# Optimization experiments

Hardware: AMD Instinct MI355X
Metric: run time of the kernel (lower is better)

The kernel has to match this reference:

```python
import jax, jax.numpy as jnp
import numpy as np

N, E, IN_C, HID, OUT_C, HEADS, NUM_CLASSES = 50000, 800000, 128, 64, 64, 4, 40
NEG_SLOPE = 0.2


def _gat_conv(x, src, dst, W, a_src, a_dst, bias, heads, concat):
    # x: [N, F_in]; W: [F_in, heads*C]; a_src/a_dst: [1, heads, C]; bias: [out]
    n = x.shape[0]
    h = (x @ W).reshape(n, heads, -1)                      # [N, H, C]
    alpha_s = (h * a_src).sum(-1)                          # [N, H]
    alpha_d = (h * a_dst).sum(-1)                          # [N, H]
    e = jax.nn.leaky_relu(alpha_s[src] + alpha_d[dst], NEG_SLOPE)  # [E, H]
    # scatter-softmax over incoming edges of each dst node
    emax = jax.ops.segment_max(e, dst, num_segments=n)
    emax = jnp.where(jnp.isfinite(emax), emax, 0.0)
    ee = jnp.exp(e - emax[dst])
    denom = jax.ops.segment_sum(ee, dst, num_segments=n) + 1e-16
    w = ee / denom[dst]                                    # [E, H]
    out = jax.ops.segment_sum(h[src] * w[:, :, None], dst, num_segments=n)  # [N, H, C]
    out = out.reshape(n, -1) if concat else out.mean(axis=1)
    return out + bias


def setup_inputs() -> dict:
    key = jax.random.key(0)
    ks = jax.random.split(key, 12)
    s1 = 1.0 / np.sqrt(IN_C)
    s2 = 1.0 / np.sqrt(HID * HEADS)
    s3 = 1.0 / np.sqrt(OUT_C)
    return {
        "x": jax.random.normal(ks[0], (N, IN_C), dtype=jnp.float32),
        "edge_index": jax.random.randint(ks[1], (2, E), 0, N, dtype=jnp.int64),
        "W1": jax.random.normal(ks[2], (IN_C, HEADS * HID), dtype=jnp.float32) * s1,
        "att_src1": jax.random.normal(ks[3], (1, HEADS, HID), dtype=jnp.float32) * s1,
        "att_dst1": jax.random.normal(ks[4], (1, HEADS, HID), dtype=jnp.float32) * s1,
        "b1": jnp.zeros((HEADS * HID,), dtype=jnp.float32),
        "W2": jax.random.normal(ks[5], (HEADS * HID, OUT_C), dtype=jnp.float32) * s2,
        "att_src2": jax.random.normal(ks[6], (1, 1, OUT_C), dtype=jnp.float32) * s2,
        "att_dst2": jax.random.normal(ks[7], (1, 1, OUT_C), dtype=jnp.float32) * s2,
        "b2": jnp.zeros((OUT_C,), dtype=jnp.float32),
        "fc_w": jax.random.normal(ks[8], (OUT_C, NUM_CLASSES), dtype=jnp.float32) * s3,
        "fc_b": jnp.zeros((NUM_CLASSES,), dtype=jnp.float32),
    }


def reference(x, edge_index, W1, att_src1, att_dst1, b1, W2, att_src2, att_dst2, b2, fc_w, fc_b):
    n = x.shape[0]
    loops = jnp.arange(n, dtype=edge_index.dtype)
    ei = jnp.concatenate([edge_index, jnp.stack([loops, loops])], axis=1)  # add self-loops (PyG default)
    src, dst = ei[0], ei[1]
    h = jax.nn.relu(_gat_conv(x, src, dst, W1, att_src1, att_dst1, b1, HEADS, True))
    h = jax.nn.relu(_gat_conv(h, src, dst, W2, att_src2, att_dst2, b2, 1, False))
    # dropout p=0.01 is identity in eval mode
    pooled = h.mean(axis=0, keepdims=True)                 # global mean pool -> [1, OUT_C]
    logits = pooled @ fc_w + fc_b
    return jax.nn.log_softmax(logits, axis=1)
```

## Files before the change

kernel.cpp:

```cpp
#include <hip/hip_runtime.h>
#include <hip/hip_bf16.h>
#include <math.h>

#define NEG_SLOPE 0.2f
#define CHUNK2 2048
#define PGROUPS 32

typedef __attribute__((ext_vector_type(8))) short bf16x8;
typedef __attribute__((ext_vector_type(4))) float f32x4;
typedef __attribute__((ext_vector_type(2))) float f32x2_t;

__device__ __forceinline__ float lrelu(float a) { return a >= 0.f ? a : NEG_SLOPE * a; }
__device__ __forceinline__ unsigned short f2bu(float v) {
  unsigned u = __float_as_uint(v);
  u += 0x7fffu + ((u >> 16) & 1u);
  return (unsigned short)(u >> 16);
}
__device__ __forceinline__ unsigned char f2fp8(float v) {
  return (unsigned char)(__builtin_amdgcn_cvt_pk_fp8_f32(v, v, 0, false) & 0xFF);
}
__device__ __forceinline__ void fp8x4_dec(unsigned v, float& a, float& b, float& c, float& d) {
  f32x2_t lo = __builtin_amdgcn_cvt_pk_f32_fp8(v, false);
  f32x2_t hi = __builtin_amdgcn_cvt_pk_f32_fp8(v, true);
  a = lo.x; b = lo.y; c = hi.x; d = hi.y;
}

__global__ __launch_bounds__(256) void prep_kernel(
    const float4* __restrict__ x4, ushort4* __restrict__ xb4, int nx4,
    const float* __restrict__ W1, unsigned short* __restrict__ w1t,
    const float* __restrict__ W2, unsigned short* __restrict__ w2t,
    const int* __restrict__ ei, int* __restrict__ bhist, int E0, int Etot, int NBUCK,
    int castBlocks, int wBlocks, int histBlocks) {
  __shared__ int hsm[256];
  int t = threadIdx.x;
  if (blockIdx.x < (unsigned)castBlocks) {
    for (int i = blockIdx.x * 256 + t; i < nx4; i += castBlocks * 256) {
      float4 v = x4[i];
      xb4[i] = make_ushort4(f2bu(v.x), f2bu(v.y), f2bu(v.z), f2bu(v.w));
    }
  } else if (blockIdx.x < (unsigned)(castBlocks + wBlocks)) {
    int bid = blockIdx.x - castBlocks;
    const int tot1 = 128 * 256, tot2 = 256 * 64;
    for (int i = bid * 256 + t; i < tot1 + tot2; i += wBlocks * 256) {
      if (i < tot1) { int k = i >> 8, n = i & 255; w1t[n * 128 + k] = f2bu(W1[i]); }
      else { int j = i - tot1; int k = j >> 6, n = j & 63; w2t[n * 256 + k] = f2bu(W2[j]); }
    }
  } else {
    int bid = blockIdx.x - castBlocks - wBlocks;
    hsm[t] = 0;
    __syncthreads();
    for (int e = bid * 256 + t; e < Etot; e += histBlocks * 256) {
      int dst = (e < E0) ? ei[E0 + e] : (e - E0);
      atomicAdd(&hsm[dst >> 8], 1);
    }
    __syncthreads();
    if (t < NBUCK && hsm[t]) atomicAdd(&bhist[t], hsm[t]);
  }
}

__global__ __launch_bounds__(256) void bucket_scan_kernel(const int* __restrict__ bhist,
    int* __restrict__ bucketOff, int* __restrict__ cursor, int* __restrict__ rowptrN,
    float* __restrict__ pooled_grp, int NBUCK, int Etot) {
  __shared__ int s[256];
  int t = threadIdx.x;
  int v = (t < NBUCK) ? bhist[t] : 0;
  s[t] = v;
  __syncthreads();
  for (int off = 1; off < 256; off <<= 1) {
    int u = (t >= off) ? s[t - off] : 0;
    __syncthreads();
    s[t] += u;
    __syncthreads();
  }
  int excl = s[t] - v;
  if (t < NBUCK) { bucketOff[t] = excl; cursor[t] = excl; }
  if (t == 0) { bucketOff[NBUCK] = Etot; *rowptrN = Etot; }
  for (int i = t; i < PGROUPS * 64; i += 256) pooled_grp[i] = 0.f;
}

__device__ void gemm_tile(const unsigned short* __restrict__ A,
    const unsigned short* __restrict__ BT, unsigned char* __restrict__ C8,
    const float* __restrict__ att_s, const float* __restrict__ att_d,
    float* __restrict__ as_, float* __restrict__ ad_,
    int M, int K, int Ncol, int H, int bx, int by, char* smem) {
  unsigned short (*Al)[40] = (unsigned short (*)[40])smem;
  unsigned short (*Bt)[40] = (unsigned short (*)[40])(smem + 5120);
  float* sal = (float*)(smem + 10240);
  float* sad = (float*)(smem + 10752);
  const int tid = threadIdx.x;
  const int row0 = by * 64, col0 = bx * 64;
  const int lane = tid & 63, wave = tid >> 6;
  const int wm = wave >> 1, wn = wave & 1;
  const int l15 = lane & 15, q = lane >> 4;

  f32x4 acc[2][2] = {};

  const int rr = tid >> 2, rc = (tid & 3) * 8;

  for (int k0 = 0; k0 < K; k0 += 32) {
    ushort4 av0 = make_ushort4(0, 0, 0, 0), av1 = av0;
    if (row0 + rr < M) {
      const ushort4* ap = (const ushort4*)(A + (size_t)(row0 + rr) * K + k0 + rc);
      av0 = ap[0]; av1 = ap[1];
    }
    *(ushort4*)&Al[rr][rc] = av0;
    *(ushort4*)&Al[rr][rc + 4] = av1;
    {
      const ushort4* bp = (const ushort4*)(BT + (size_t)(col0 + rr) * K + k0 + rc);
      *(ushort4*)&Bt[rr][rc] = bp[0];
      *(ushort4*)&Bt[rr][rc + 4] = bp[1];
    }
    __syncthreads();
    bf16x8 af[2], bf[2];
#pragma unroll
    for (int mi = 0; mi < 2; mi++)
      af[mi] = *(const bf16x8*)&Al[wm * 32 + mi * 16 + l15][q * 8];
#pragma unroll
    for (int ni = 0; ni < 2; ni++)
      bf[ni] = *(const bf16x8*)&Bt[wn * 32 + ni * 16 + l15][q * 8];
#pragma unroll
    for (int mi = 0; mi < 2; mi++)
#pragma unroll
      for (int ni = 0; ni < 2; ni++)
        acc[mi][ni] = __builtin_amdgcn_mfma_f32_16x16x32_bf16(af[mi], bf[ni], acc[mi][ni], 0, 0, 0);
    __syncthreads();
  }
#pragma unroll
  for (int mi = 0; mi < 2; mi++) {
#pragma unroll
    for (int r = 0; r < 4; r++) {
      int grow = row0 + wm * 32 + mi * 16 + q * 4 + r;
      if (grow < M) {
#pragma unroll
        for (int ni = 0; ni < 2; ni++) {
          int gcol = col0 + wn * 32 + ni * 16 + l15;
          C8[(size_t)grow * Ncol + gcol] = f2fp8(acc[mi][ni][r]);
        }
      }
    }
  }
  float atts0 = att_s[col0 + wn * 32 + l15];
  float atts1 = att_s[col0 + wn * 32 + 16 + l15];
  float attd0 = att_d[col0 + wn * 32 + l15];
  float attd1 = att_d[col0 + wn * 32 + 16 + l15];
#pragma unroll
  for (int mi = 0; mi < 2; mi++) {
#pragma unroll
    for (int r = 0; r < 4; r++) {
      float vs = acc[mi][0][r] * atts0 + acc[mi][1][r] * atts1;
      float vd = acc[mi][0][r] * attd0 + acc[mi][1][r] * attd1;
#pragma unroll
      for (int off = 1; off < 16; off <<= 1) {
        vs += __shfl_xor(vs, off);
        vd += __shfl_xor(vd, off);
      }
      if (l15 == 0) {
        int rl = wm * 32 + mi * 16 + q * 4 + r;
        sal[wn * 64 + rl] = vs;
        sad[wn * 64 + rl] = vd;
      }
    }
  }
  __syncthreads();
  if (tid < 64) {
    int grow = row0 + tid;
    if (grow < M) {
      as_[(size_t)grow * H + bx] = sal[tid] + sal[64 + tid];
      ad_[(size_t)grow * H + bx] = sad[tid] + sad[64 + tid];
    }
  }
}

__global__ __launch_bounds__(256) void gemm_alpha_kernel(const unsigned short* __restrict__ A,
    const unsigned short* __restrict__ BT, unsigned char* __restrict__ C8,
    const float* __restrict__ att_s, const float* __restrict__ att_d,
    float* __restrict__ as_, float* __restrict__ ad_, int M, int K, int Ncol, int H) {
  __shared__ __align__(16) char smem[11264];
  gemm_tile(A, BT, C8, att_s, att_d, as_, ad_, M, K, Ncol, H, blockIdx.x, blockIdx.y, smem);
}

__global__ __launch_bounds__(256) void gemm1_scatter_kernel(
    const unsigned short* __restrict__ A, const unsigned short* __restrict__ BT,
    unsigned char* __restrict__ C8, const float* __restrict__ att_s,
    const float* __restrict__ att_d, float* __restrict__ as_, float* __restrict__ ad_,
    int M, int K, int Ncol, int H, int GX,
    const int* __restrict__ ei, int* __restrict__ cursor, int* __restrict__ pairs,
    int E0, int Etot, int NBUCK, int NSC) {
  __shared__ __align__(16) char smem[18432];
  if (blockIdx.x < (unsigned)NSC) {
    int2* stage = (int2*)smem;
    int* h = (int*)(smem + 16384);
    int* base = (int*)(smem + 17408);
    int t = threadIdx.x;
    int e0 = blockIdx.x * CHUNK2;
    h[t] = 0;
    __syncthreads();
    int cnt = Etot - e0;
    if (cnt > CHUNK2) cnt = CHUNK2;
    for (int i = t; i < cnt; i += 256) {
      int e = e0 + i;
      int s, d;
      if (e < E0) { s = ei[e]; d = ei[E0 + e]; } else { s = d = e - E0; }
      stage[i] = make_int2((s << 8) | (d & 255), d >> 8);
      atomicAdd(&h[d >> 8], 1);
    }
    __syncthreads();
    if (t < NBUCK && h[t]) base[t] = atomicAdd(&cursor[t], h[t]);
    __syncthreads();
    for (int i = t; i < cnt; i += 256) {
      int2 p = stage[i];
      int pos = atomicAdd(&base[p.y], 1);
      pairs[pos] = p.x;
    }
  } else {
    int flat = blockIdx.x - NSC;
    gemm_tile(A, BT, C8, att_s, att_d, as_, ad_, M, K, Ncol, H, flat % GX, flat / GX, smem);
  }
}

__global__ __launch_bounds__(256) void csr_build_kernel(const int* __restrict__ pairs,
    const int* __restrict__ bucketOff, int* __restrict__ rowptr, int* __restrict__ csr_src,
    int N) {
  int b = blockIdx.x, t = threadIdx.x;
  int base = bucketOff[b], cnt = bucketOff[b + 1] - base;
  int n0 = b << 8;
  __shared__ int h[256];
  __shared__ int s[256];
  __shared__ int ex[256];
  h[t] = 0;
  __syncthreads();
  for (int i = t; i < cnt; i += 256) atomicAdd(&h[pairs[base + i] & 255], 1);
  __syncthreads();
  int v = h[t];
  s[t] = v;
  __syncthreads();
  for (int off = 1; off < 256; off <<= 1) {
    int u = (t >= off) ? s[t - off] : 0;
    __syncthreads();
    s[t] += u;
    __syncthreads();
  }
  ex[t] = s[t] - v;
  if (n0 + t < N) rowptr[n0 + t] = base + ex[t];
  __syncthreads();
  for (int i = t; i < cnt; i += 256) {
    int p = pairs[base + i];
    int pos = atomicAdd(&ex[p & 255], 1);
    csr_src[base + pos] = ((unsigned)p) >> 8;
  }
}

#define ACC16(W, X) do {                                                       \
    float c0_, c1_, c2_, c3_;                                                  \
    fp8x4_dec((X).x, c0_, c1_, c2_, c3_);                                      \
    acc[0] = fmaf((W), c0_, acc[0]);  acc[1] = fmaf((W), c1_, acc[1]);         \
    acc[2] = fmaf((W), c2_, acc[2]);  acc[3] = fmaf((W), c3_, acc[3]);         \
    fp8x4_dec((X).y, c0_, c1_, c2_, c3_);                                      \
    acc[4] = fmaf((W), c0_, acc[4]);  acc[5] = fmaf((W), c1_, acc[5]);         \
    acc[6] = fmaf((W), c2_, acc[6]);  acc[7] = fmaf((W), c3_, acc[7]);         \
    fp8x4_dec((X).z, c0_, c1_, c2_, c3_);                                      \
    acc[8] = fmaf((W), c0_, acc[8]);  acc[9] = fmaf((W), c1_, acc[9]);         \
    acc[10] = fmaf((W), c2_, acc[10]); acc[11] = fmaf((W), c3_, acc[11]);      \
    fp8x4_dec((X).w, c0_, c1_, c2_, c3_);                                      \
    acc[12] = fmaf((W), c0_, acc[12]); acc[13] = fmaf((W), c1_, acc[13]);      \
    acc[14] = fmaf((W), c2_, acc[14]); acc[15] = fmaf((W), c3_, acc[15]);      \
  } while (0)

__global__ __launch_bounds__(256) void aggr1_kernel(const int* __restrict__ rowptr,
    const int* __restrict__ csr_src, const float* __restrict__ as_,
    const float* __restrict__ ad_, const uint4* __restrict__ h1f8,
    const float* __restrict__ b1, unsigned short* __restrict__ out1, int Nn) {
  int lane = threadIdx.x & 63, wv = threadIdx.x >> 6;
  int q = lane >> 4, l15 = lane & 15;
  int n = (blockIdx.x * 4 + wv) * 4 + q;
  if (n >= Nn) return;
  int row = rowptr[n], deg = rowptr[n + 1] - row;
  int rowEnd = row + deg;
  int hh = l15 >> 2;
  float adv = ad_[n * 4 + hh];
  const uint4* hb = h1f8 + l15;
  float acc[16] = {};
  float wsum = 0.f;
  int p0 = row + l15;
  int idxv = (p0 < rowEnd) ? csr_src[p0] : 0;
  for (int s0 = 0; s0 < deg; s0 += 16) {
    int pn = row + s0 + 16 + l15;
    int idxn = (pn < rowEnd) ? csr_src[pn] : 0;
    int m = deg - s0;
    if (m > 16) m = 16;
    int j = 0;
    for (; j + 4 <= m; j += 4) {
      int i0 = __shfl(idxv, j, 16);
      int i1 = __shfl(idxv, j + 1, 16);
      int i2 = __shfl(idxv, j + 2, 16);
      int i3 = __shfl(idxv, j + 3, 16);
      float a0v = as_[i0 * 4 + hh];
      float a1v = as_[i1 * 4 + hh];
      float a2v = as_[i2 * 4 + hh];
      float a3v = as_[i3 * 4 + hh];
      uint4 x0 = hb[(size_t)i0 * 16];
      uint4 x1 = hb[(size_t)i1 * 16];
      uint4 x2 = hb[(size_t)i2 * 16];
      uint4 x3 = hb[(size_t)i3 * 16];
      float w0 = __expf(lrelu(a0v + adv));
      float w1 = __expf(lrelu(a1v + adv));
      float w2 = __expf(lrelu(a2v + adv));
      float w3 = __expf(lrelu(a3v + adv));
      wsum += (w0 + w1) + (w2 + w3);
      ACC16(w0, x0);
      ACC16(w1, x1);
      ACC16(w2, x2);
      ACC16(w3, x3);
    }
    for (; j < m; j++) {
      int i0 = __shfl(idxv, j, 16);
      float a0v = as_[i0 * 4 + hh];
      uint4 x0 = hb[(size_t)i0 * 16];
      float w0 = __expf(lrelu(a0v + adv));
      wsum += w0;
      ACC16(w0, x0);
    }
    idxv = idxn;
  }
  float vinv = 1.f / wsum;
  int c0i = l15 * 16;
  unsigned short ob[16];
#pragma unroll
  for (int k = 0; k < 4; k++) {
    float4 bb = *(const float4*)(b1 + c0i + k * 4);
    float r0 = fmaf(acc[k * 4 + 0], vinv, bb.x);
    float r1 = fmaf(acc[k * 4 + 1], vinv, bb.y);
    float r2 = fmaf(acc[k * 4 + 2], vinv, bb.z);
    float r3 = fmaf(acc[k * 4 + 3], vinv, bb.w);
    ob[k * 4 + 0] = f2bu(r0 > 0.f ? r0 : 0.f);
    ob[k * 4 + 1] = f2bu(r1 > 0.f ? r1 : 0.f);
    ob[k * 4 + 2] = f2bu(r2 > 0.f ? r2 : 0.f);
    ob[k * 4 + 3] = f2bu(r3 > 0.f ? r3 : 0.f);
  }
  *(ushort4*)(out1 + (size_t)n * 256 + c0i) = *(ushort4*)&ob[0];
  *(ushort4*)(out1 + (size_t)n * 256 + c0i + 4) = *(ushort4*)&ob[4];
  *(ushort4*)(out1 + (size_t)n * 256 + c0i + 8) = *(ushort4*)&ob[8];
  *(ushort4*)(out1 + (size_t)n * 256 + c0i + 12) = *(ushort4*)&ob[12];
}

__global__ __launch_bounds__(256) void aggr2_pool_kernel(const int* __restrict__ rowptr,
    const int* __restrict__ csr_src, const float* __restrict__ as_,
    const float* __restrict__ ad_, const unsigned* __restrict__ h2f8,
    const float* __restrict__ b2, float* __restrict__ pooled_grp, int Nn) {
  int lane = threadIdx.x & 63, wv = threadIdx.x >> 6;
  int q = lane >> 4, l15 = lane & 15;
  int c0 = l15 * 4;
  const unsigned* hb = h2f8 + l15;
  float p0 = 0.f, p1 = 0.f, p2 = 0.f, p3 = 0.f;
  int stream = (blockIdx.x * 4 + wv) * 4 + q;
  int nstreams = gridDim.x * 16;
  for (int n = stream; n < Nn; n += nstreams) {
    int row = rowptr[n], deg = rowptr[n + 1] - row;
    int rowEnd = row + deg;
    float adv = ad_[n];
    float a0 = 0.f, a1 = 0.f, a2 = 0.f, a3 = 0.f, wsum = 0.f;
    int pp = row + l15;
    int idxv = (pp < rowEnd) ? csr_src[pp] : 0;
    for (int s0 = 0; s0 < deg; s0 += 16) {
      int pn = row + s0 + 16 + l15;
      int idxn = (pn < rowEnd) ? csr_src[pn] : 0;
      int m = deg - s0;
      if (m > 16) m = 16;
      int j = 0;
      for (; j + 8 <= m; j += 8) {
        int id[8];
        float al[8];
        unsigned xv[8];
#pragma unroll
        for (int u = 0; u < 8; u++) id[u] = __shfl(idxv, j + u, 16);
#pragma unroll
        for (int u = 0; u < 8; u++) al[u] = as_[id[u]];
#pragma unroll
        for (int u = 0; u < 8; u++) xv[u] = hb[(size_t)id[u] * 16];
#pragma unroll
        for (int u = 0; u < 8; u++) {
          float w = __expf(lrelu(al[u] + adv));
          wsum += w;
          float c0f, c1f, c2f, c3f;
          fp8x4_dec(xv[u], c0f, c1f, c2f, c3f);
          a0 = fmaf(w, c0f, a0); a1 = fmaf(w, c1f, a1);
          a2 = fmaf(w, c2f, a2); a3 = fmaf(w, c3f, a3);
        }
      }
      for (; j + 4 <= m; j += 4) {
        int id[4];
        float al[4];
        unsigned xv[4];
#pragma unroll
        for (int u = 0; u < 4; u++) id[u] = __shfl(idxv, j + u, 16);
#pragma unroll
        for (int u = 0; u < 4; u++) al[u] = as_[id[u]];
#pragma unroll
        for (int u = 0; u < 4; u++) xv[u] = hb[(size_t)id[u] * 16];
#pragma unroll
        for (int u = 0; u < 4; u++) {
          float w = __expf(lrelu(al[u] + adv));
          wsum += w;
          float c0f, c1f, c2f, c3f;
          fp8x4_dec(xv[u], c0f, c1f, c2f, c3f);
          a0 = fmaf(w, c0f, a0); a1 = fmaf(w, c1f, a1);
          a2 = fmaf(w, c2f, a2); a3 = fmaf(w, c3f, a3);
        }
      }
      for (; j < m; j++) {
        int i0 = __shfl(idxv, j, 16);
        float w = __expf(lrelu(as_[i0] + adv));
        wsum += w;
        float c0f, c1f, c2f, c3f;
        fp8x4_dec(hb[(size_t)i0 * 16], c0f, c1f, c2f, c3f);
        a0 = fmaf(w, c0f, a0); a1 = fmaf(w, c1f, a1);
        a2 = fmaf(w, c2f, a2); a3 = fmaf(w, c3f, a3);
      }
      idxv = idxn;
    }
    float vinv = 1.f / wsum;
    float4 bb = *(const float4*)(b2 + c0);
    float r0 = fmaf(a0, vinv, bb.x), r1 = fmaf(a1, vinv, bb.y);
    float r2 = fmaf(a2, vinv, bb.z), r3 = fmaf(a3, vinv, bb.w);
    p0 += r0 > 0.f ? r0 : 0.f; p1 += r1 > 0.f ? r1 : 0.f;
    p2 += r2 > 0.f ? r2 : 0.f; p3 += r3 > 0.f ? r3 : 0.f;
  }
  __shared__ float4 sred[4][4][16];
  sred[wv][q][l15] = make_float4(p0, p1, p2, p3);
  __syncthreads();
  if (threadIdx.x < 64) {
    int slot = threadIdx.x >> 2, comp = threadIdx.x & 3;
    float acc = 0.f;
#pragma unroll
    for (int i = 0; i < 4; i++)
#pragma unroll
      for (int j = 0; j < 4; j++) {
        float4 v = sred[i][j][slot];
        acc += comp == 0 ? v.x : (comp == 1 ? v.y : (comp == 2 ? v.z : v.w));
      }
    atomicAdd(&pooled_grp[(blockIdx.x & (PGROUPS - 1)) * 64 + slot * 4 + comp], acc);
  }
}

__global__ __launch_bounds__(64) void pool_head_kernel(const float* __restrict__ pooled_grp,
    const float* __restrict__ fc_w, const float* __restrict__ fc_b,
    float* __restrict__ out, float invN) {
  int t = threadIdx.x;
  __shared__ float pl[64];
  __shared__ float lg[40];
  __shared__ float lse;
  float acc = 0.f;
#pragma unroll
  for (int g = 0; g < PGROUPS; g++) acc += pooled_grp[g * 64 + t];
  pl[t] = acc * invN;
  __syncthreads();
  if (t < 40) {
    float sm = fc_b[t];
    for (int c = 0; c < 64; c++) sm = fmaf(pl[c], fc_w[c * 40 + t], sm);
    lg[t] = sm;
  }
  __syncthreads();
  if (t == 0) {
    float m = -1e30f;
    for (int j = 0; j < 40; j++) m = fmaxf(m, lg[j]);
    float su = 0.f;
    for (int j = 0; j < 40; j++) su += expf(lg[j] - m);
    lse = m + logf(su);
  }
  __syncthreads();
  if (t < 40) out[t] = lg[t] - lse;
}

extern "C" void kernel_launch(void* const* d_in, const int* in_sizes, int n_in,
                              void* d_out, int out_size, void* d_ws, size_t ws_size,
                              hipStream_t stream) {
  const float* x        = (const float*)d_in[0];
  const int*   ei       = (const int*)d_in[1];
  const float* W1       = (const float*)d_in[2];
  const float* att_src1 = (const float*)d_in[3];
  const float* att_dst1 = (const float*)d_in[4];
  const float* b1       = (const float*)d_in[5];
  const float* W2       = (const float*)d_in[6];
  const float* att_src2 = (const float*)d_in[7];
  const float* att_dst2 = (const float*)d_in[8];
  const float* b2       = (const float*)d_in[9];
  const float* fc_w     = (const float*)d_in[10];
  const float* fc_b     = (const float*)d_in[11];
  float* out = (float*)d_out;

  const int N    = in_sizes[0] / 128;
  const int E0   = in_sizes[1] / 2;
  const int Etot = E0 + N;
  const int NBUCK = (N + 255) >> 8;
  const int NSC  = (Etot + CHUNK2 - 1) / CHUNK2;
  const int GBY  = (N + 63) / 64;
  const int AGG2_BLOCKS = 2048;

  char* wsb = (char*)d_ws;
  size_t o = 0;
  auto alloc = [&](size_t bytes) { char* p = wsb + o; o += (bytes + 15) & ~(size_t)15; return p; };
  unsigned short* xb   = (unsigned short*)alloc((size_t)N * 128 * 2);
  unsigned short* w1t  = (unsigned short*)alloc(256 * 128 * 2);
  unsigned short* w2t  = (unsigned short*)alloc(64 * 256 * 2);
  unsigned char*  h1f8 = (unsigned char*)alloc((size_t)N * 256);
  unsigned short* out1 = (unsigned short*)alloc((size_t)N * 256 * 2);
  float* as1  = (float*)alloc((size_t)N * 4 * 4);
  float* ad1  = (float*)alloc((size_t)N * 4 * 4);
  float* as2  = (float*)alloc((size_t)N * 4);
  float* ad2  = (float*)alloc((size_t)N * 4);
  int* rowptr = (int*)alloc((size_t)(N + 1) * 4);
  int* bhist  = (int*)alloc(256 * 4);
  int* bucketOff = (int*)alloc(257 * 4);
  int* cursor = (int*)alloc(256 * 4);
  int* pairs  = (int*)alloc((size_t)Etot * 4);
  int* csr_src = (int*)alloc((size_t)Etot * 4);
  float* pooled_grp = (float*)alloc((size_t)PGROUPS * 64 * 4);

  dim3 blk(256);

  hipMemsetAsync(bhist, 0, 256 * sizeof(int), stream);
  prep_kernel<<<512 + 16 + 256, blk, 0, stream>>>(
      (const float4*)x, (ushort4*)xb, N * 128 / 4,
      W1, w1t, W2, w2t,
      ei, bhist, E0, Etot, NBUCK, 512, 16, 256);
  bucket_scan_kernel<<<1, blk, 0, stream>>>(bhist, bucketOff, cursor, rowptr + N,
                                            pooled_grp, NBUCK, Etot);

  gemm1_scatter_kernel<<<NSC + 4 * GBY, blk, 0, stream>>>(
      xb, w1t, h1f8, att_src1, att_dst1, as1, ad1, N, 128, 256, 4, 4,
      ei, cursor, pairs, E0, Etot, NBUCK, NSC);
  csr_build_kernel<<<NBUCK, blk, 0, stream>>>(pairs, bucketOff, rowptr, csr_src, N);

  aggr1_kernel<<<(N + 15) / 16, blk, 0, stream>>>(rowptr, csr_src, as1, ad1,
                                                  (const uint4*)h1f8, b1, out1, N);

  gemm_alpha_kernel<<<dim3(1, GBY), blk, 0, stream>>>(out1, w2t, h1f8, att_src2, att_dst2,
                                                      as2, ad2, N, 256, 64, 1);
  aggr2_pool_kernel<<<AGG2_BLOCKS, blk, 0, stream>>>(rowptr, csr_src, as2, ad2,
                                                     (const unsigned*)h1f8, b2, pooled_grp, N);

  pool_head_kernel<<<1, 64, 0, stream>>>(pooled_grp, fc_w, fc_b, out, 1.0f / (float)N);
}
```

Before: 221.7 us.

## Fuse x cast into GEMM1, merge bucket scan into prep, restructure GEMMs

Drops the separate fp32-to-bf16 cast of x and has GEMM1 load x directly and convert it in-tile. GEMM1 now computes a full 64x256 row tile per block with W1 fully resident in swizzled LDS, and writes the per-head alpha values directly. The bucket scan kernel is folded into prep_kernel through a last-block-done atomic counter, and GEMM2 becomes a single-pass kernel with the whole K dimension staged in LDS. The goal is fewer launches and less global traffic, at the cost of large LDS use (80KB per block in the fused scatter kernel), which limits occupancy, including for the scatter blocks.

```diff
diff --git a/kernel.cpp b/kernel.cpp
--- a/kernel.cpp
+++ b/kernel.cpp
@@ -26,27 +26,23 @@
 }
 
 __global__ __launch_bounds__(256) void prep_kernel(
-    const float4* __restrict__ x4, ushort4* __restrict__ xb4, int nx4,
     const float* __restrict__ W1, unsigned short* __restrict__ w1t,
     const float* __restrict__ W2, unsigned short* __restrict__ w2t,
-    const int* __restrict__ ei, int* __restrict__ bhist, int E0, int Etot, int NBUCK,
-    int castBlocks, int wBlocks, int histBlocks) {
+    const int* __restrict__ ei, int* __restrict__ bhist, int* __restrict__ done,
+    int* __restrict__ bucketOff, int* __restrict__ cursor, int* __restrict__ rowptrN,
+    float* __restrict__ pooled_grp,
+    int E0, int Etot, int NBUCK, int wBlocks, int histBlocks) {
   __shared__ int hsm[256];
+  __shared__ int rank;
   int t = threadIdx.x;
-  if (blockIdx.x < (unsigned)castBlocks) {
-    for (int i = blockIdx.x * 256 + t; i < nx4; i += castBlocks * 256) {
-      float4 v = x4[i];
-      xb4[i] = make_ushort4(f2bu(v.x), f2bu(v.y), f2bu(v.z), f2bu(v.w));
-    }
-  } else if (blockIdx.x < (unsigned)(castBlocks + wBlocks)) {
-    int bid = blockIdx.x - castBlocks;
+  if (blockIdx.x < (unsigned)wBlocks) {
     const int tot1 = 128 * 256, tot2 = 256 * 64;
-    for (int i = bid * 256 + t; i < tot1 + tot2; i += wBlocks * 256) {
+    for (int i = blockIdx.x * 256 + t; i < tot1 + tot2; i += wBlocks * 256) {
       if (i < tot1) { int k = i >> 8, n = i & 255; w1t[n * 128 + k] = f2bu(W1[i]); }
       else { int j = i - tot1; int k = j >> 6, n = j & 63; w2t[n * 256 + k] = f2bu(W2[j]); }
     }
   } else {
-    int bid = blockIdx.x - castBlocks - wBlocks;
+    int bid = blockIdx.x - wBlocks;
     hsm[t] = 0;
     __syncthreads();
     for (int e = bid * 256 + t; e < Etot; e += histBlocks * 256) {
@@ -55,138 +51,124 @@
     }
     __syncthreads();
     if (t < NBUCK && hsm[t]) atomicAdd(&bhist[t], hsm[t]);
-  }
-}
-
-__global__ __launch_bounds__(256) void bucket_scan_kernel(const int* __restrict__ bhist,
-    int* __restrict__ bucketOff, int* __restrict__ cursor, int* __restrict__ rowptrN,
-    float* __restrict__ pooled_grp, int NBUCK, int Etot) {
-  __shared__ int s[256];
-  int t = threadIdx.x;
-  int v = (t < NBUCK) ? bhist[t] : 0;
-  s[t] = v;
-  __syncthreads();
-  for (int off = 1; off < 256; off <<= 1) {
-    int u = (t >= off) ? s[t - off] : 0;
-    __syncthreads();
-    s[t] += u;
-    __syncthreads();
-  }
-  int excl = s[t] - v;
-  if (t < NBUCK) { bucketOff[t] = excl; cursor[t] = excl; }
-  if (t == 0) { bucketOff[NBUCK] = Etot; *rowptrN = Etot; }
-  for (int i = t; i < PGROUPS * 64; i += 256) pooled_grp[i] = 0.f;
-}
-
-__device__ void gemm_tile(const unsigned short* __restrict__ A,
-    const unsigned short* __restrict__ BT, unsigned char* __restrict__ C8,
+    __threadfence();
+    if (t == 0) rank = atomicAdd(done, 1);
+    __syncthreads();
+    if (rank == histBlocks - 1) {
+      int v = (t < NBUCK) ? atomicAdd(&bhist[t], 0) : 0;
+      __syncthreads();
+      hsm[t] = v;
+      __syncthreads();
+      for (int off = 1; off < 256; off <<= 1) {
+        int u = (t >= off) ? hsm[t - off] : 0;
+        __syncthreads();
+        hsm[t] += u;
+        __syncthreads();
+      }
+      int excl = hsm[t] - v;
+      if (t < NBUCK) { bucketOff[t] = excl; cursor[t] = excl; }
+      if (t == 0) { bucketOff[NBUCK] = Etot; *rowptrN = Etot; }
+      for (int i = t; i < PGROUPS * 64; i += 256) pooled_grp[i] = 0.f;
+    }
+  }
+}
+
+__device__ void gemm1_tile(const float* __restrict__ x,
+    const unsigned short* __restrict__ w1t, unsigned char* __restrict__ C8,
     const float* __restrict__ att_s, const float* __restrict__ att_d,
-    float* __restrict__ as_, float* __restrict__ ad_,
-    int M, int K, int Ncol, int H, int bx, int by, char* smem) {
-  unsigned short (*Al)[40] = (unsigned short (*)[40])smem;
-  unsigned short (*Bt)[40] = (unsigned short (*)[40])(smem + 5120);
-  float* sal = (float*)(smem + 10240);
-  float* sad = (float*)(smem + 10752);
-  const int tid = threadIdx.x;
-  const int row0 = by * 64, col0 = bx * 64;
-  const int lane = tid & 63, wave = tid >> 6;
-  const int wm = wave >> 1, wn = wave & 1;
+    float* __restrict__ as_, float* __restrict__ ad_, int M, int by, char* smem) {
+  const int t = threadIdx.x;
+  const int row0 = by * 64;
+  const int lane = t & 63, wave = t >> 6;
   const int l15 = lane & 15, q = lane >> 4;
-
-  f32x4 acc[2][2] = {};
-
-  const int rr = tid >> 2, rc = (tid & 3) * 8;
-
-  for (int k0 = 0; k0 < K; k0 += 32) {
-    ushort4 av0 = make_ushort4(0, 0, 0, 0), av1 = av0;
-    if (row0 + rr < M) {
-      const ushort4* ap = (const ushort4*)(A + (size_t)(row0 + rr) * K + k0 + rc);
-      av0 = ap[0]; av1 = ap[1];
-    }
-    *(ushort4*)&Al[rr][rc] = av0;
-    *(ushort4*)&Al[rr][rc + 4] = av1;
-    {
-      const ushort4* bp = (const ushort4*)(BT + (size_t)(col0 + rr) * K + k0 + rc);
-      *(ushort4*)&Bt[rr][rc] = bp[0];
-      *(ushort4*)&Bt[rr][rc + 4] = bp[1];
-    }
-    __syncthreads();
-    bf16x8 af[2], bf[2];
-#pragma unroll
-    for (int mi = 0; mi < 2; mi++)
-      af[mi] = *(const bf16x8*)&Al[wm * 32 + mi * 16 + l15][q * 8];
-#pragma unroll
-    for (int ni = 0; ni < 2; ni++)
-      bf[ni] = *(const bf16x8*)&Bt[wn * 32 + ni * 16 + l15][q * 8];
-#pragma unroll
-    for (int mi = 0; mi < 2; mi++)
-#pragma unroll
-      for (int ni = 0; ni < 2; ni++)
+  char* Bs = smem;
+  char* As = smem + 65536;
+
+  {
+    const uint4* src = (const uint4*)w1t;
+#pragma unroll
+    for (int i = 0; i < 16; i++) {
+      int c = t + 256 * i;
+      int row = c >> 4, bc = (c & 15) << 4;
+      *(uint4*)(Bs + row * 256 + (bc ^ ((row & 7) << 4))) = src[c];
+    }
+  }
+  {
+#pragma unroll
+    for (int i = 0; i < 8; i++) {
+      int c = t + 256 * i;
+      int row = c >> 5, fc = (c & 31) << 2;
+      float4 v = make_float4(0.f, 0.f, 0.f, 0.f);
+      if (row0 + row < M) v = *(const float4*)(x + (size_t)(row0 + row) * 128 + fc);
+      ushort4 b = make_ushort4(f2bu(v.x), f2bu(v.y), f2bu(v.z), f2bu(v.w));
+      int bc = (c & 31) << 3;
+      *(ushort4*)(As + row * 256 + (bc ^ ((row & 7) << 4))) = b;
+    }
+  }
+  __syncthreads();
+
+  f32x4 acc[4][4] = {};
+  for (int k0 = 0; k0 < 128; k0 += 32) {
+    int kb = k0 * 2 + q * 16;
+    bf16x8 af[4], bf[4];
+#pragma unroll
+    for (int mi = 0; mi < 4; mi++) {
+      int row = mi * 16 + l15;
+      af[mi] = *(const bf16x8*)(As + row * 256 + (kb ^ ((row & 7) << 4)));
+    }
+#pragma unroll
+    for (int ni = 0; ni < 4; ni++) {
+      int row = wave * 64 + ni * 16 + l15;
+      bf[ni] = *(const bf16x8*)(Bs + row * 256 + (kb ^ ((row & 7) << 4)));
+    }
+#pragma unroll
+    for (int mi = 0; mi < 4; mi++)
+#pragma unroll
+      for (int ni = 0; ni < 4; ni++)
         acc[mi][ni] = __builtin_amdgcn_mfma_f32_16x16x32_bf16(af[mi], bf[ni], acc[mi][ni], 0, 0, 0);
-    __syncthreads();
-  }
-#pragma unroll
-  for (int mi = 0; mi < 2; mi++) {
+  }
+
+  float atts[4], attd[4];
+#pragma unroll
+  for (int ni = 0; ni < 4; ni++) {
+    atts[ni] = att_s[wave * 64 + ni * 16 + l15];
+    attd[ni] = att_d[wave * 64 + ni * 16 + l15];
+  }
+#pragma unroll
+  for (int mi = 0; mi < 4; mi++) {
 #pragma unroll
     for (int r = 0; r < 4; r++) {
-      int grow = row0 + wm * 32 + mi * 16 + q * 4 + r;
-      if (grow < M) {
-#pragma unroll
-        for (int ni = 0; ni < 2; ni++) {
-          int gcol = col0 + wn * 32 + ni * 16 + l15;
-          C8[(size_t)grow * Ncol + gcol] = f2fp8(acc[mi][ni][r]);
-        }
-      }
-    }
-  }
-  float atts0 = att_s[col0 + wn * 32 + l15];
-  float atts1 = att_s[col0 + wn * 32 + 16 + l15];
-  float attd0 = att_d[col0 + wn * 32 + l15];
-  float attd1 = att_d[col0 + wn * 32 + 16 + l15];
-#pragma unroll
-  for (int mi = 0; mi < 2; mi++) {
-#pragma unroll
-    for (int r = 0; r < 4; r++) {
-      float vs = acc[mi][0][r] * atts0 + acc[mi][1][r] * atts1;
-      float vd = acc[mi][0][r] * attd0 + acc[mi][1][r] * attd1;
+      int grow = row0 + mi * 16 + q * 4 + r;
+      bool ok = grow < M;
+      if (ok) {
+#pragma unroll
+        for (int ni = 0; ni < 4; ni++)
+          C8[(size_t)grow * 256 + wave * 64 + ni * 16 + l15] = f2fp8(acc[mi][ni][r]);
+      }
+      float vs = acc[mi][0][r] * atts[0] + acc[mi][1][r] * atts[1]
+               + acc[mi][2][r] * atts[2] + acc[mi][3][r] * atts[3];
+      float vd = acc[mi][0][r] * attd[0] + acc[mi][1][r] * attd[1]
+               + acc[mi][2][r] * attd[2] + acc[mi][3][r] * attd[3];
 #pragma unroll
       for (int off = 1; off < 16; off <<= 1) {
         vs += __shfl_xor(vs, off);
         vd += __shfl_xor(vd, off);
       }
-      if (l15 == 0) {
-        int rl = wm * 32 + mi * 16 + q * 4 + r;
-        sal[wn * 64 + rl] = vs;
-        sad[wn * 64 + rl] = vd;
-      }
-    }
-  }
-  __syncthreads();
-  if (tid < 64) {
-    int grow = row0 + tid;
-    if (grow < M) {
-      as_[(size_t)grow * H + bx] = sal[tid] + sal[64 + tid];
-      ad_[(size_t)grow * H + bx] = sad[tid] + sad[64 + tid];
-    }
-  }
-}
-
-__global__ __launch_bounds__(256) void gemm_alpha_kernel(const unsigned short* __restrict__ A,
-    const unsigned short* __restrict__ BT, unsigned char* __restrict__ C8,
-    const float* __restrict__ att_s, const float* __restrict__ att_d,
-    float* __restrict__ as_, float* __restrict__ ad_, int M, int K, int Ncol, int H) {
-  __shared__ __align__(16) char smem[11264];
-  gemm_tile(A, BT, C8, att_s, att_d, as_, ad_, M, K, Ncol, H, blockIdx.x, blockIdx.y, smem);
+      if (ok && l15 == 0) {
+        as_[(size_t)grow * 4 + wave] = vs;
+        ad_[(size_t)grow * 4 + wave] = vd;
+      }
+    }
+  }
 }
 
 __global__ __launch_bounds__(256) void gemm1_scatter_kernel(
-    const unsigned short* __restrict__ A, const unsigned short* __restrict__ BT,
+    const float* __restrict__ x, const unsigned short* __restrict__ w1t,
     unsigned char* __restrict__ C8, const float* __restrict__ att_s,
     const float* __restrict__ att_d, float* __restrict__ as_, float* __restrict__ ad_,
-    int M, int K, int Ncol, int H, int GX,
-    const int* __restrict__ ei, int* __restrict__ cursor, int* __restrict__ pairs,
+    int M, const int* __restrict__ ei, int* __restrict__ cursor, int* __restrict__ pairs,
     int E0, int Etot, int NBUCK, int NSC) {
-  __shared__ __align__(16) char smem[18432];
+  __shared__ __align__(16) char smem[81920];
   if (blockIdx.x < (unsigned)NSC) {
     int2* stage = (int2*)smem;
     int* h = (int*)(smem + 16384);
@@ -213,8 +195,102 @@
       pairs[pos] = p.x;
     }
   } else {
-    int flat = blockIdx.x - NSC;
-    gemm_tile(A, BT, C8, att_s, att_d, as_, ad_, M, K, Ncol, H, flat % GX, flat / GX, smem);
+    gemm1_tile(x, w1t, C8, att_s, att_d, as_, ad_, M, blockIdx.x - NSC, smem);
+  }
+}
+
+__global__ __launch_bounds__(256) void gemm2_kernel(const unsigned short* __restrict__ out1,
+    const unsigned short* __restrict__ w2t, unsigned char* __restrict__ C8,
+    const float* __restrict__ att_s, const float* __restrict__ att_d,
+    float* __restrict__ as_, float* __restrict__ ad_, int M) {
+  __shared__ __align__(16) char smem[66560];
+  const int t = threadIdx.x;
+  const int row0 = blockIdx.x * 64;
+  const int lane = t & 63, wave = t >> 6;
+  const int wm = wave >> 1, wn = wave & 1;
+  const int l15 = lane & 15, q = lane >> 4;
+  char* As = smem;
+  char* Bs = smem + 32768;
+  float* sal = (float*)(smem + 65536);
+  float* sad = (float*)(smem + 66048);
+
+#pragma unroll
+  for (int i = 0; i < 8; i++) {
+    int c = t + 256 * i;
+    int row = c >> 5, bc = (c & 31) << 4;
+    uint4 v = make_uint4(0, 0, 0, 0);
+    if (row0 + row < M) v = *(const uint4*)(out1 + (size_t)(row0 + row) * 256 + ((c & 31) << 3));
+    *(uint4*)(As + row * 512 + (bc ^ ((row & 7) << 4))) = v;
+  }
+#pragma unroll
+  for (int i = 0; i < 8; i++) {
+    int c = t + 256 * i;
+    int row = c >> 5, bc = (c & 31) << 4;
+    uint4 v = *(const uint4*)(w2t + ((size_t)c << 3));
+    *(uint4*)(Bs + row * 512 + (bc ^ ((row & 7) << 4))) = v;
+  }
+  __syncthreads();
+
+  f32x4 acc[2][2] = {};
+  for (int k0 = 0; k0 < 256; k0 += 32) {
+    int kb = k0 * 2 + q * 16;
+    bf16x8 af[2], bf[2];
+#pragma unroll
+    for (int mi = 0; mi < 2; mi++) {
+      int row = wm * 32 + mi * 16 + l15;
+      af[mi] = *(const bf16x8*)(As + row * 512 + (kb ^ ((row & 7) << 4)));
+    }
+#pragma unroll
+    for (int ni = 0; ni < 2; ni++) {
+      int row = wn * 32 + ni * 16 + l15;
+      bf[ni] = *(const bf16x8*)(Bs + row * 512 + (kb ^ ((row & 7) << 4)));
+    }
+#pragma unroll
+    for (int mi = 0; mi < 2; mi++)
+#pragma unroll
+      for (int ni = 0; ni < 2; ni++)
+        acc[mi][ni] = __builtin_amdgcn_mfma_f32_16x16x32_bf16(af[mi], bf[ni], acc[mi][ni], 0, 0, 0);
+  }
+
+#pragma unroll
+  for (int mi = 0; mi < 2; mi++) {
+#pragma unroll
+    for (int r = 0; r < 4; r++) {
+      int grow = row0 + wm * 32 + mi * 16 + q * 4 + r;
+      if (grow < M) {
+#pragma unroll
+        for (int ni = 0; ni < 2; ni++)
+          C8[(size_t)grow * 64 + wn * 32 + ni * 16 + l15] = f2fp8(acc[mi][ni][r]);
+      }
+    }
+  }
+  float atts0 = att_s[wn * 32 + l15], atts1 = att_s[wn * 32 + 16 + l15];
+  float attd0 = att_d[wn * 32 + l15], attd1 = att_d[wn * 32 + 16 + l15];
+#pragma unroll
+  for (int mi = 0; mi < 2; mi++) {
+#pragma unroll
+    for (int r = 0; r < 4; r++) {
+      float vs = acc[mi][0][r] * atts0 + acc[mi][1][r] * atts1;
+      float vd = acc[mi][0][r] * attd0 + acc[mi][1][r] * attd1;
+#pragma unroll
+      for (int off = 1; off < 16; off <<= 1) {
+        vs += __shfl_xor(vs, off);
+        vd += __shfl_xor(vd, off);
+      }
+      if (l15 == 0) {
+        int rl = wm * 32 + mi * 16 + q * 4 + r;
+        sal[wn * 64 + rl] = vs;
+        sad[wn * 64 + rl] = vd;
+      }
+    }
+  }
+  __syncthreads();
+  if (t < 64) {
+    int grow = row0 + t;
+    if (grow < M) {
+      as_[grow] = sal[t] + sal[64 + t];
+      ad_[grow] = sad[t] + sad[64 + t];
+    }
   }
 }
 
@@ -499,7 +575,6 @@
   char* wsb = (char*)d_ws;
   size_t o = 0;
   auto alloc = [&](size_t bytes) { char* p = wsb + o; o += (bytes + 15) & ~(size_t)15; return p; };
-  unsigned short* xb   = (unsigned short*)alloc((size_t)N * 128 * 2);
   unsigned short* w1t  = (unsigned short*)alloc(256 * 128 * 2);
   unsigned short* w2t  = (unsigned short*)alloc(64 * 256 * 2);
   unsigned char*  h1f8 = (unsigned char*)alloc((size_t)N * 256);
@@ -509,33 +584,30 @@
   float* as2  = (float*)alloc((size_t)N * 4);
   float* ad2  = (float*)alloc((size_t)N * 4);
   int* rowptr = (int*)alloc((size_t)(N + 1) * 4);
-  int* bhist  = (int*)alloc(256 * 4);
+  int* bhist  = (int*)alloc(260 * 4);
   int* bucketOff = (int*)alloc(257 * 4);
   int* cursor = (int*)alloc(256 * 4);
   int* pairs  = (int*)alloc((size_t)Etot * 4);
   int* csr_src = (int*)alloc((size_t)Etot * 4);
   float* pooled_grp = (float*)alloc((size_t)PGROUPS * 64 * 4);
+  int* done = bhist + 256;
 
   dim3 blk(256);
 
-  hipMemsetAsync(bhist, 0, 256 * sizeof(int), stream);
-  prep_kernel<<<512 + 16 + 256, blk, 0, stream>>>(
-      (const float4*)x, (ushort4*)xb, N * 128 / 4,
-      W1, w1t, W2, w2t,
-      ei, bhist, E0, Etot, NBUCK, 512, 16, 256);
-  bucket_scan_kernel<<<1, blk, 0, stream>>>(bhist, bucketOff, cursor, rowptr + N,
-                                            pooled_grp, NBUCK, Etot);
-
-  gemm1_scatter_kernel<<<NSC + 4 * GBY, blk, 0, stream>>>(
-      xb, w1t, h1f8, att_src1, att_dst1, as1, ad1, N, 128, 256, 4, 4,
+  hipMemsetAsync(bhist, 0, 257 * sizeof(int), stream);
+  prep_kernel<<<16 + 256, blk, 0, stream>>>(
+      W1, w1t, W2, w2t, ei, bhist, done, bucketOff, cursor, rowptr + N, pooled_grp,
+      E0, Etot, NBUCK, 16, 256);
+
+  gemm1_scatter_kernel<<<NSC + GBY, blk, 0, stream>>>(
+      x, w1t, h1f8, att_src1, att_dst1, as1, ad1, N,
       ei, cursor, pairs, E0, Etot, NBUCK, NSC);
   csr_build_kernel<<<NBUCK, blk, 0, stream>>>(pairs, bucketOff, rowptr, csr_src, N);
 
   aggr1_kernel<<<(N + 15) / 16, blk, 0, stream>>>(rowptr, csr_src, as1, ad1,
                                                   (const uint4*)h1f8, b1, out1, N);
 
-  gemm_alpha_kernel<<<dim3(1, GBY), blk, 0, stream>>>(out1, w2t, h1f8, att_src2, att_dst2,
-                                                      as2, ad2, N, 256, 64, 1);
+  gemm2_kernel<<<GBY, blk, 0, stream>>>(out1, w2t, h1f8, att_src2, att_dst2, as2, ad2, N);
   aggr2_pool_kernel<<<AGG2_BLOCKS, blk, 0, stream>>>(rowptr, csr_src, as2, ad2,
                                                      (const unsigned*)h1f8, b2, pooled_grp, N);
 
```

Measured after the change: 241.0 us. 1.09x slower.

## Fuse layer-2 GEMM into aggregation, fold x cast into GEMM1, merge scan

Applied to the files above, without the earlier changes.

The layer-1 aggregation kernel now writes its 16-node bf16 output tile into swizzled shared memory and immediately runs the layer-2 MFMA projection plus attention dot products, removing the out1 round trip and the separate gemm_alpha launch. The x-to-bf16 cast is moved into the GEMM1 tile load, eliminating the xb buffer and cast blocks. The bucket scan is merged into the histogram kernel via a last-block-done atomic counter, removing one launch. The fused aggregation kernel carries more shared memory and registers, which may lower occupancy, and the last-block pattern depends on fences being correct.

```diff
diff --git a/kernel.cpp b/kernel.cpp
--- a/kernel.cpp
+++ b/kernel.cpp
@@ -26,27 +26,23 @@
 }
 
 __global__ __launch_bounds__(256) void prep_kernel(
-    const float4* __restrict__ x4, ushort4* __restrict__ xb4, int nx4,
     const float* __restrict__ W1, unsigned short* __restrict__ w1t,
     const float* __restrict__ W2, unsigned short* __restrict__ w2t,
-    const int* __restrict__ ei, int* __restrict__ bhist, int E0, int Etot, int NBUCK,
-    int castBlocks, int wBlocks, int histBlocks) {
+    const int* __restrict__ ei, int* __restrict__ bhist, int* __restrict__ done,
+    int* __restrict__ bucketOff, int* __restrict__ cursor, int* __restrict__ rowptrN,
+    float* __restrict__ pooled_grp,
+    int E0, int Etot, int NBUCK, int wBlocks, int histBlocks) {
   __shared__ int hsm[256];
+  __shared__ int rank;
   int t = threadIdx.x;
-  if (blockIdx.x < (unsigned)castBlocks) {
-    for (int i = blockIdx.x * 256 + t; i < nx4; i += castBlocks * 256) {
-      float4 v = x4[i];
-      xb4[i] = make_ushort4(f2bu(v.x), f2bu(v.y), f2bu(v.z), f2bu(v.w));
-    }
-  } else if (blockIdx.x < (unsigned)(castBlocks + wBlocks)) {
-    int bid = blockIdx.x - castBlocks;
+  if (blockIdx.x < (unsigned)wBlocks) {
     const int tot1 = 128 * 256, tot2 = 256 * 64;
-    for (int i = bid * 256 + t; i < tot1 + tot2; i += wBlocks * 256) {
+    for (int i = blockIdx.x * 256 + t; i < tot1 + tot2; i += wBlocks * 256) {
       if (i < tot1) { int k = i >> 8, n = i & 255; w1t[n * 128 + k] = f2bu(W1[i]); }
       else { int j = i - tot1; int k = j >> 6, n = j & 63; w2t[n * 256 + k] = f2bu(W2[j]); }
     }
   } else {
-    int bid = blockIdx.x - castBlocks - wBlocks;
+    int bid = blockIdx.x - wBlocks;
     hsm[t] = 0;
     __syncthreads();
     for (int e = bid * 256 + t; e < Etot; e += histBlocks * 256) {
@@ -55,34 +51,34 @@
     }
     __syncthreads();
     if (t < NBUCK && hsm[t]) atomicAdd(&bhist[t], hsm[t]);
-  }
-}
-
-__global__ __launch_bounds__(256) void bucket_scan_kernel(const int* __restrict__ bhist,
-    int* __restrict__ bucketOff, int* __restrict__ cursor, int* __restrict__ rowptrN,
-    float* __restrict__ pooled_grp, int NBUCK, int Etot) {
-  __shared__ int s[256];
-  int t = threadIdx.x;
-  int v = (t < NBUCK) ? bhist[t] : 0;
-  s[t] = v;
-  __syncthreads();
-  for (int off = 1; off < 256; off <<= 1) {
-    int u = (t >= off) ? s[t - off] : 0;
-    __syncthreads();
-    s[t] += u;
-    __syncthreads();
-  }
-  int excl = s[t] - v;
-  if (t < NBUCK) { bucketOff[t] = excl; cursor[t] = excl; }
-  if (t == 0) { bucketOff[NBUCK] = Etot; *rowptrN = Etot; }
-  for (int i = t; i < PGROUPS * 64; i += 256) pooled_grp[i] = 0.f;
-}
-
-__device__ void gemm_tile(const unsigned short* __restrict__ A,
+    __threadfence();
+    if (t == 0) rank = atomicAdd(done, 1);
+    __syncthreads();
+    if (rank == histBlocks - 1) {
+      int v = (t < NBUCK) ? atomicAdd(&bhist[t], 0) : 0;
+      __syncthreads();
+      hsm[t] = v;
+      __syncthreads();
+      for (int off = 1; off < 256; off <<= 1) {
+        int u = (t >= off) ? hsm[t - off] : 0;
+        __syncthreads();
+        hsm[t] += u;
+        __syncthreads();
+      }
+      int excl = hsm[t] - v;
+      if (t < NBUCK) { bucketOff[t] = excl; cursor[t] = excl; }
+      if (t == 0) { bucketOff[NBUCK] = Etot; *rowptrN = Etot; }
+      for (int i = t; i < PGROUPS * 64; i += 256) pooled_grp[i] = 0.f;
+    }
+  }
+}
+
+__device__ void gemm1_tile(const float* __restrict__ x,
     const unsigned short* __restrict__ BT, unsigned char* __restrict__ C8,
     const float* __restrict__ att_s, const float* __restrict__ att_d,
     float* __restrict__ as_, float* __restrict__ ad_,
-    int M, int K, int Ncol, int H, int bx, int by, char* smem) {
+    int M, int bx, int by, char* smem) {
+  const int K = 128;
   unsigned short (*Al)[40] = (unsigned short (*)[40])smem;
   unsigned short (*Bt)[40] = (unsigned short (*)[40])(smem + 5120);
   float* sal = (float*)(smem + 10240);
@@ -98,13 +94,14 @@
   const int rr = tid >> 2, rc = (tid & 3) * 8;
 
   for (int k0 = 0; k0 < K; k0 += 32) {
-    ushort4 av0 = make_ushort4(0, 0, 0, 0), av1 = av0;
+    float4 v0 = make_float4(0.f, 0.f, 0.f, 0.f), v1 = v0;
     if (row0 + rr < M) {
-      const ushort4* ap = (const ushort4*)(A + (size_t)(row0 + rr) * K + k0 + rc);
-      av0 = ap[0]; av1 = ap[1];
-    }
-    *(ushort4*)&Al[rr][rc] = av0;
-    *(ushort4*)&Al[rr][rc + 4] = av1;
+      const float* ap = x + (size_t)(row0 + rr) * K + k0 + rc;
+      v0 = *(const float4*)ap;
+      v1 = *(const float4*)(ap + 4);
+    }
+    *(ushort4*)&Al[rr][rc] = make_ushort4(f2bu(v0.x), f2bu(v0.y), f2bu(v0.z), f2bu(v0.w));
+    *(ushort4*)&Al[rr][rc + 4] = make_ushort4(f2bu(v1.x), f2bu(v1.y), f2bu(v1.z), f2bu(v1.w));
     {
       const ushort4* bp = (const ushort4*)(BT + (size_t)(col0 + rr) * K + k0 + rc);
       *(ushort4*)&Bt[rr][rc] = bp[0];
@@ -134,7 +131,7 @@
 #pragma unroll
         for (int ni = 0; ni < 2; ni++) {
           int gcol = col0 + wn * 32 + ni * 16 + l15;
-          C8[(size_t)grow * Ncol + gcol] = f2fp8(acc[mi][ni][r]);
+          C8[(size_t)grow * 256 + gcol] = f2fp8(acc[mi][ni][r]);
         }
       }
     }
@@ -165,26 +162,17 @@
   if (tid < 64) {
     int grow = row0 + tid;
     if (grow < M) {
-      as_[(size_t)grow * H + bx] = sal[tid] + sal[64 + tid];
-      ad_[(size_t)grow * H + bx] = sad[tid] + sad[64 + tid];
-    }
-  }
-}
-
-__global__ __launch_bounds__(256) void gemm_alpha_kernel(const unsigned short* __restrict__ A,
-    const unsigned short* __restrict__ BT, unsigned char* __restrict__ C8,
-    const float* __restrict__ att_s, const float* __restrict__ att_d,
-    float* __restrict__ as_, float* __restrict__ ad_, int M, int K, int Ncol, int H) {
-  __shared__ __align__(16) char smem[11264];
-  gemm_tile(A, BT, C8, att_s, att_d, as_, ad_, M, K, Ncol, H, blockIdx.x, blockIdx.y, smem);
+      as_[(size_t)grow * 4 + bx] = sal[tid] + sal[64 + tid];
+      ad_[(size_t)grow * 4 + bx] = sad[tid] + sad[64 + tid];
+    }
+  }
 }
 
 __global__ __launch_bounds__(256) void gemm1_scatter_kernel(
-    const unsigned short* __restrict__ A, const unsigned short* __restrict__ BT,
+    const float* __restrict__ x, const unsigned short* __restrict__ BT,
     unsigned char* __restrict__ C8, const float* __restrict__ att_s,
     const float* __restrict__ att_d, float* __restrict__ as_, float* __restrict__ ad_,
-    int M, int K, int Ncol, int H, int GX,
-    const int* __restrict__ ei, int* __restrict__ cursor, int* __restrict__ pairs,
+    int M, const int* __restrict__ ei, int* __restrict__ cursor, int* __restrict__ pairs,
     int E0, int Etot, int NBUCK, int NSC) {
   __shared__ __align__(16) char smem[18432];
   if (blockIdx.x < (unsigned)NSC) {
@@ -214,7 +202,7 @@
     }
   } else {
     int flat = blockIdx.x - NSC;
-    gemm_tile(A, BT, C8, att_s, att_d, as_, ad_, M, K, Ncol, H, flat % GX, flat / GX, smem);
+    gemm1_tile(x, BT, C8, att_s, att_d, as_, ad_, M, flat % 4, flat / 4, smem);
   }
 }
 
@@ -266,18 +254,26 @@
     acc[14] = fmaf((W), c2_, acc[14]); acc[15] = fmaf((W), c3_, acc[15]);      \
   } while (0)
 
-__global__ __launch_bounds__(256) void aggr1_kernel(const int* __restrict__ rowptr,
+__global__ __launch_bounds__(256) void aggr1_gemm2_kernel(const int* __restrict__ rowptr,
     const int* __restrict__ csr_src, const float* __restrict__ as_,
     const float* __restrict__ ad_, const uint4* __restrict__ h1f8,
-    const float* __restrict__ b1, unsigned short* __restrict__ out1, int Nn) {
+    const float* __restrict__ b1, const unsigned short* __restrict__ w2t,
+    const float* __restrict__ att_s2, const float* __restrict__ att_d2,
+    unsigned char* __restrict__ h2, float* __restrict__ as2, float* __restrict__ ad2,
+    int Nn) {
+  __shared__ __align__(16) char As[16 * 512];
+  __shared__ float sal[64], sad[64];
   int lane = threadIdx.x & 63, wv = threadIdx.x >> 6;
   int q = lane >> 4, l15 = lane & 15;
-  int n = (blockIdx.x * 4 + wv) * 4 + q;
-  if (n >= Nn) return;
-  int row = rowptr[n], deg = rowptr[n + 1] - row;
+  int nloc = wv * 4 + q;
+  int base = blockIdx.x * 16;
+  int n = base + nloc;
+  bool active = n < Nn;
+  int row = 0, deg = 0;
+  if (active) { row = rowptr[n], deg = rowptr[n + 1] - row; }
   int rowEnd = row + deg;
   int hh = l15 >> 2;
-  float adv = ad_[n * 4 + hh];
+  float adv = active ? ad_[n * 4 + hh] : 0.f;
   const uint4* hb = h1f8 + l15;
   float acc[16] = {};
   float wsum = 0.f;
@@ -322,7 +318,7 @@
     }
     idxv = idxn;
   }
-  float vinv = 1.f / wsum;
+  float vinv = (deg > 0) ? 1.f / wsum : 0.f;
   int c0i = l15 * 16;
   unsigned short ob[16];
 #pragma unroll
@@ -337,10 +333,46 @@
     ob[k * 4 + 2] = f2bu(r2 > 0.f ? r2 : 0.f);
     ob[k * 4 + 3] = f2bu(r3 > 0.f ? r3 : 0.f);
   }
-  *(ushort4*)(out1 + (size_t)n * 256 + c0i) = *(ushort4*)&ob[0];
-  *(ushort4*)(out1 + (size_t)n * 256 + c0i + 4) = *(ushort4*)&ob[4];
-  *(ushort4*)(out1 + (size_t)n * 256 + c0i + 8) = *(ushort4*)&ob[8];
-  *(ushort4*)(out1 + (size_t)n * 256 + c0i + 12) = *(ushort4*)&ob[12];
+#pragma unroll
+  for (int j = 0; j < 4; j++)
+    *(ushort4*)(As + nloc * 512 + ((l15 * 32 + j * 8) ^ ((nloc & 7) << 4))) =
+        *(ushort4*)&ob[j * 4];
+  __syncthreads();
+
+  bf16x8 bfr[8];
+#pragma unroll
+  for (int k = 0; k < 8; k++)
+    bfr[k] = *(const bf16x8*)(w2t + (size_t)(wv * 16 + l15) * 256 + k * 32 + q * 8);
+  f32x4 acc2 = {};
+#pragma unroll
+  for (int k = 0; k < 8; k++) {
+    bf16x8 af = *(const bf16x8*)(As + l15 * 512 + ((k * 64 + q * 16) ^ ((l15 & 7) << 4)));
+    acc2 = __builtin_amdgcn_mfma_f32_16x16x32_bf16(af, bfr[k], acc2, 0, 0, 0);
+  }
+  float atts = att_s2[wv * 16 + l15], attd = att_d2[wv * 16 + l15];
+#pragma unroll
+  for (int r = 0; r < 4; r++) {
+    int node = q * 4 + r;
+    int grow = base + node;
+    if (grow < Nn) h2[(size_t)grow * 64 + wv * 16 + l15] = f2fp8(acc2[r]);
+    float vs = acc2[r] * atts;
+    float vd = acc2[r] * attd;
+#pragma unroll
+    for (int off = 1; off < 16; off <<= 1) {
+      vs += __shfl_xor(vs, off);
+      vd += __shfl_xor(vd, off);
+    }
+    if (l15 == 0) {
+      sal[wv * 16 + node] = vs;
+      sad[wv * 16 + node] = vd;
+    }
+  }
+  __syncthreads();
+  if (threadIdx.x < 16 && base + (int)threadIdx.x < Nn) {
+    int t = threadIdx.x;
+    as2[base + t] = sal[t] + sal[16 + t] + sal[32 + t] + sal[48 + t];
+    ad2[base + t] = sad[t] + sad[16 + t] + sad[32 + t] + sad[48 + t];
+  }
 }
 
 __global__ __launch_bounds__(256) void aggr2_pool_kernel(const int* __restrict__ rowptr,
@@ -499,45 +531,41 @@
   char* wsb = (char*)d_ws;
   size_t o = 0;
   auto alloc = [&](size_t bytes) { char* p = wsb + o; o += (bytes + 15) & ~(size_t)15; return p; };
-  unsigned short* xb   = (unsigned short*)alloc((size_t)N * 128 * 2);
   unsigned short* w1t  = (unsigned short*)alloc(256 * 128 * 2);
   unsigned short* w2t  = (unsigned short*)alloc(64 * 256 * 2);
   unsigned char*  h1f8 = (unsigned char*)alloc((size_t)N * 256);
-  unsigned short* out1 = (unsigned short*)alloc((size_t)N * 256 * 2);
+  unsigned char*  h2   = (unsigned char*)alloc((size_t)N * 64);
   float* as1  = (float*)alloc((size_t)N * 4 * 4);
   float* ad1  = (float*)alloc((size_t)N * 4 * 4);
   float* as2  = (float*)alloc((size_t)N * 4);
   float* ad2  = (float*)alloc((size_t)N * 4);
   int* rowptr = (int*)alloc((size_t)(N + 1) * 4);
-  int* bhist  = (int*)alloc(256 * 4);
+  int* bhist  = (int*)alloc(260 * 4);
   int* bucketOff = (int*)alloc(257 * 4);
   int* cursor = (int*)alloc(256 * 4);
   int* pairs  = (int*)alloc((size_t)Etot * 4);
   int* csr_src = (int*)alloc((size_t)Etot * 4);
   float* pooled_grp = (float*)alloc((size_t)PGROUPS * 64 * 4);
+  int* done = bhist + 256;
 
   dim3 blk(256);
 
-  hipMemsetAsync(bhist, 0, 256 * sizeof(int), stream);
-  prep_kernel<<<512 + 16 + 256, blk, 0, stream>>>(
-      (const float4*)x, (ushort4*)xb, N * 128 / 4,
-      W1, w1t, W2, w2t,
-      ei, bhist, E0, Etot, NBUCK, 512, 16, 256);
-  bucket_scan_kernel<<<1, blk, 0, stream>>>(bhist, bucketOff, cursor, rowptr + N,
-                                            pooled_grp, NBUCK, Etot);
+  hipMemsetAsync(bhist, 0, 257 * sizeof(int), stream);
+  prep_kernel<<<16 + 256, blk, 0, stream>>>(
+      W1, w1t, W2, w2t, ei, bhist, done, bucketOff, cursor, rowptr + N, pooled_grp,
+      E0, Etot, NBUCK, 16, 256);
 
   gemm1_scatter_kernel<<<NSC + 4 * GBY, blk, 0, stream>>>(
-      xb, w1t, h1f8, att_src1, att_dst1, as1, ad1, N, 128, 256, 4, 4,
+      x, w1t, h1f8, att_src1, att_dst1, as1, ad1, N,
       ei, cursor, pairs, E0, Etot, NBUCK, NSC);
   csr_build_kernel<<<NBUCK, blk, 0, stream>>>(pairs, bucketOff, rowptr, csr_src, N);
 
-  aggr1_kernel<<<(N + 15) / 16, blk, 0, stream>>>(rowptr, csr_src, as1, ad1,
-                                                  (const uint4*)h1f8, b1, out1, N);
-
-  gemm_alpha_kernel<<<dim3(1, GBY), blk, 0, stream>>>(out1, w2t, h1f8, att_src2, att_dst2,
-                                                      as2, ad2, N, 256, 64, 1);
+  aggr1_gemm2_kernel<<<(N + 15) / 16, blk, 0, stream>>>(
+      rowptr, csr_src, as1, ad1, (const uint4*)h1f8, b1, w2t, att_src2, att_dst2,
+      h2, as2, ad2, N);
+
   aggr2_pool_kernel<<<AGG2_BLOCKS, blk, 0, stream>>>(rowptr, csr_src, as2, ad2,
-                                                     (const unsigned*)h1f8, b2, pooled_grp, N);
+                                                     (const unsigned*)h2, b2, pooled_grp, N);
 
   pool_head_kernel<<<1, 64, 0, stream>>>(pooled_grp, fc_w, fc_b, out, 1.0f / (float)N);
 }
```

Result: slower. 243.2 us (+9.7%).
